# Performance work log

Hardware: AMD Instinct MI355X
Metric: run time of the kernel (lower is better)

Reference implementation:

```python
import jax, jax.numpy as jnp
import numpy as np


def setup_inputs() -> dict:
    key = jax.random.key(0)
    k1, k2, k3, k4 = jax.random.split(key, 4)
    B, I, P, F = 4096, 1024, 512, 2048
    x = jax.random.normal(k1, (B, I), dtype=jnp.float32)
    # params initialized like torch.rand(...)*2-1 (uniform in [-1,1])
    features = jax.random.uniform(k2, (F, I), dtype=jnp.float32, minval=-1.0, maxval=1.0)
    prototypes = jax.random.uniform(k3, (P, I), dtype=jnp.float32, minval=-1.0, maxval=1.0)
    # scalars: torch inits to zeros; use small nonzero values so output/grads are informative
    abt = jax.random.normal(k4, (3,), dtype=jnp.float32) * 0.1
    alpha = abt[0:1]
    beta = abt[1:2]
    theta = abt[2:3]
    return {"x": x, "features": features, "prototypes": prototypes,
            "alpha": alpha, "beta": beta, "theta": theta}


def reference(x, features, prototypes, alpha, beta, theta):
    # x: [b, i], features: [f, i], prototypes: [p, i]
    # Original einsums broadcast over p but the projection is p-independent:
    xf = x @ features.T            # [b, f]
    pf = prototypes @ features.T   # [p, f]
    x_pres = jax.nn.relu(xf)       # [b, f]
    p_pres = jax.nn.relu(pf)       # [p, f]
    # common[b,p]       = sum_f xf*pf*relu(xf)*relu(pf)
    # x_distinct[b,p]   = sum_f xf*relu(xf)*(1-relu(pf))
    # p_distinct[b,p]   = sum_f pf*relu(pf)*(1-relu(xf))
    a = xf * x_pres                # [b, f]
    c = pf * p_pres                # [p, f]
    common = a @ c.T                                   # [b, p]
    x_distinctive = a @ (1.0 - p_pres).T               # [b, p]
    p_distinctive = (1.0 - x_pres) @ c.T               # [b, p]
    return theta * common - alpha * x_distinctive - beta * p_distinctive
```

## Files before the change

### kernel.cpp

```cpp
#include <hip/hip_runtime.h>
#include <cstdint>

typedef __attribute__((ext_vector_type(8))) short bf16x8;
typedef __attribute__((ext_vector_type(4))) float f32x4;
typedef __attribute__((ext_vector_type(4))) float f4;
typedef __attribute__((ext_vector_type(4))) unsigned short u16x4;
typedef __attribute__((ext_vector_type(8))) unsigned short u16x8;
typedef unsigned short u16;

__device__ __forceinline__ u16 f2bf(float f) {
  uint32_t u = __builtin_bit_cast(uint32_t, f);
  u += 0x7fffu + ((u >> 16) & 1u);
  return (u16)(u >> 16);
}

__device__ __forceinline__ void async_cp16(const void* g, void* l) {
  __builtin_amdgcn_global_load_lds(
      (const __attribute__((address_space(1))) uint32_t*)g,
      (__attribute__((address_space(3))) uint32_t*)l, 16, 0, 0);
}

__global__ __launch_bounds__(256) void cast3(
    const float* __restrict__ x, const float* __restrict__ f,
    const float* __restrict__ p, u16* __restrict__ dst,
    int n1, int n2, int n3) {
  int i = (blockIdx.x * 256 + threadIdx.x) * 4;
  const float* src;
  int local;
  if (i < n1) { src = x; local = i; }
  else if (i < n1 + n2) { src = f; local = i - n1; }
  else if (i < n1 + n2 + n3) { src = p; local = i - n1 - n2; }
  else return;
  f4 v = *(const f4*)(src + local);
  u16x4 o;
  o.x = f2bf(v.x); o.y = f2bf(v.y); o.z = f2bf(v.z); o.w = f2bf(v.w);
  *(u16x4*)(dst + i) = o;
}

template<int TM, int TN>
__device__ __forceinline__ void mainloop(
    const u16* __restrict__ A, const u16* __restrict__ B, int K,
    int kbeg, int kend, int tid, u16* lds, f32x4 (&acc)[TM / 32][TN / 32]) {
  constexpr int BK = 64;
  constexpr int WM = TM / 2, WN = TN / 2;
  constexpr int MT = TM / 32, NT = TN / 32;
  const int lane = tid & 63;
  const int wave = tid >> 6;
  const int wrow = wave >> 1, wcol = wave & 1;

  for (int k0 = kbeg; k0 < kend; k0 += BK) {
    #pragma unroll
    for (int it = 0; it < TM / 32; ++it) {
      int c = it * 256 + tid;
      int row = c >> 3, pc = c & 7;
      int gc = pc ^ (row & 7);
      async_cp16(A + (size_t)row * K + (k0 + gc * 8),
                 &lds[(it * 256 + wave * 64) * 8]);
    }
    #pragma unroll
    for (int it = 0; it < TN / 32; ++it) {
      int c = it * 256 + tid;
      int row = c >> 3, pc = c & 7;
      int gc = pc ^ (row & 7);
      async_cp16(B + (size_t)row * K + (k0 + gc * 8),
                 &lds[TM * BK + (it * 256 + wave * 64) * 8]);
    }
    __syncthreads();

    #pragma unroll
    for (int s = 0; s < 2; ++s) {
      const int h = s * 4 + (lane >> 4);
      bf16x8 afr[MT], bfr[NT];
      #pragma unroll
      for (int i = 0; i < MT; ++i) {
        int r = wrow * WM + i * 16 + (lane & 15);
        afr[i] = *(const bf16x8*)&lds[(r * 8 + (h ^ (r & 7))) * 8];
      }
      #pragma unroll
      for (int j = 0; j < NT; ++j) {
        int r = wcol * WN + j * 16 + (lane & 15);
        bfr[j] = *(const bf16x8*)&lds[TM * BK + (r * 8 + (h ^ (r & 7))) * 8];
      }
      #pragma unroll
      for (int i = 0; i < MT; ++i)
        #pragma unroll
        for (int j = 0; j < NT; ++j)
          acc[i][j] = __builtin_amdgcn_mfma_f32_16x16x32_bf16(afr[i], bfr[j], acc[i][j], 0, 0, 0);
    }
    __syncthreads();
  }
}

__global__ __launch_bounds__(256) void gemm12(
    const u16* __restrict__ xb, const u16* __restrict__ pb,
    const u16* __restrict__ fb, u16* __restrict__ Acat, u16* __restrict__ Bcat,
    const float* __restrict__ alpha, const float* __restrict__ beta,
    const float* __restrict__ theta) {
  constexpr int TM = 128, TN = 64, K = 1024, N = 2048;
  constexpr int MT = TM / 32, NT = TN / 32;
  constexpr int TSTRIDE = 72;
  __shared__ u16 lds[(TM + TN) * 64];

  const int tid = threadIdx.x;
  const int lane = tid & 63;
  const int wave = tid >> 6;
  const int wrow = wave >> 1, wcol = wave & 1;
  const int bm_all = blockIdx.x * TM;
  const int bn = blockIdx.y * TN;
  const bool is_x = bm_all < 4096;
  const u16* A = is_x ? xb + (size_t)bm_all * K : pb + (size_t)(bm_all - 4096) * K;
  const u16* B = fb + (size_t)bn * K;

  f32x4 acc[MT][NT] = {};
  mainloop<TM, TN>(A, B, K, 0, K, tid, lds, acc);

  float th = 0.f, al = 0.f, be = 0.f;
  if (!is_x) { th = theta[0]; al = alpha[0]; be = beta[0]; }
  u16* dst = is_x ? Acat : Bcat;
  const int rowbase = is_x ? bm_all : bm_all - 4096;

  #pragma unroll
  for (int half = 0; half < 2; ++half) {
    __syncthreads();
    #pragma unroll
    for (int i = 0; i < MT; ++i) {
      #pragma unroll
      for (int j = 0; j < NT; ++j) {
        const int cl = wcol * 32 + j * 16 + (lane & 15);
        #pragma unroll
        for (int r = 0; r < 4; ++r) {
          const int rl = wrow * 64 + i * 16 + (lane >> 4) * 4 + r;
          float v = acc[i][j][r];
          float pres = v > 0.f ? v : 0.f;
          float o;
          if (is_x) o = half == 0 ? v * pres : 1.f - pres;
          else {
            float cc = v * pres;
            o = half == 0 ? th * cc - al * (1.f - pres) : -be * cc;
          }
          lds[rl * TSTRIDE + cl] = f2bf(o);
        }
      }
    }
    __syncthreads();
    #pragma unroll
    for (int v = 0; v < 4; ++v) {
      const int rl = v * 32 + (tid >> 3);
      const int cl = (tid & 7) * 8;
      u16x8 vec = *(const u16x8*)&lds[rl * TSTRIDE + cl];
      *(u16x8*)&dst[(size_t)(rowbase + rl) * (2 * N) + bn + cl + half * N] = vec;
    }
  }
}

__global__ __launch_bounds__(256) void gemm3(
    const u16* __restrict__ Acat, const u16* __restrict__ Bcat,
    float* __restrict__ part) {
  constexpr int TM = 128, TN = 64, K = 4096, KSPLIT = 4;
  constexpr int MT = TM / 32, NT = TN / 32;
  __shared__ u16 lds[(TM + TN) * 64];

  const int tid = threadIdx.x;
  const int bm = blockIdx.x * TM;
  const int bn = blockIdx.y * TN;
  const int kbeg = blockIdx.z * (K / KSPLIT);
  const int kend = kbeg + (K / KSPLIT);

  f32x4 acc[MT][NT] = {};
  mainloop<TM, TN>(Acat + (size_t)bm * K, Bcat + (size_t)bn * K, K, kbeg, kend,
                   tid, lds, acc);

  const size_t pbase =
      ((size_t)blockIdx.z * 256 + blockIdx.y * 32 + blockIdx.x) * 8192;
  #pragma unroll
  for (int i = 0; i < MT; ++i)
    #pragma unroll
    for (int j = 0; j < NT; ++j)
      *(f4*)&part[pbase + (i * NT + j) * 1024 + tid * 4] = acc[i][j];
}

__global__ __launch_bounds__(256) void reduce4(
    const float* __restrict__ part, float* __restrict__ out) {
  constexpr int N = 512;
  const int tid = threadIdx.x;
  const int lane = tid & 63;
  const int wave = tid >> 6;
  const int wrow = wave >> 1, wcol = wave & 1;
  const int tileId = blockIdx.x;
  const int bm = (tileId & 31) * 128;
  const int bn = (tileId >> 5) * 64;

  #pragma unroll
  for (int s = 0; s < 8; ++s) {
    f4 v = {0.f, 0.f, 0.f, 0.f};
    #pragma unroll
    for (int z = 0; z < 4; ++z)
      v += *(const f4*)&part[((size_t)z * 256 + tileId) * 8192 + s * 1024 + tid * 4];
    const int i = s >> 1, j = s & 1;
    const int gr0 = bm + wrow * 64 + i * 16 + (lane >> 4) * 4;
    const int gc = bn + wcol * 32 + j * 16 + (lane & 15);
    out[(size_t)(gr0 + 0) * N + gc] = v.x;
    out[(size_t)(gr0 + 1) * N + gc] = v.y;
    out[(size_t)(gr0 + 2) * N + gc] = v.z;
    out[(size_t)(gr0 + 3) * N + gc] = v.w;
  }
}

extern "C" void kernel_launch(void* const* d_in, const int* in_sizes, int n_in,
                              void* d_out, int out_size, void* d_ws, size_t ws_size,
                              hipStream_t stream) {
  const float* x     = (const float*)d_in[0];
  const float* feat  = (const float*)d_in[1];
  const float* proto = (const float*)d_in[2];
  const float* alpha = (const float*)d_in[3];
  const float* beta  = (const float*)d_in[4];
  const float* theta = (const float*)d_in[5];
  float* out = (float*)d_out;

  constexpr int Bb = 4096, Ii = 1024, Pp = 512, Ff = 2048;

  char* ws = (char*)d_ws;
  u16* xb    = (u16*)ws;
  u16* fb    = xb + (size_t)Bb * Ii;
  u16* pb    = fb + (size_t)Ff * Ii;
  float* part = (float*)ws;
  size_t r0 = (size_t)4 * 256 * 8192 * 4;
  u16* Acat = (u16*)(ws + r0);
  u16* Bcat = Acat + (size_t)Bb * 2 * Ff;

  const int n1 = Bb * Ii, n2 = Ff * Ii, n3 = Pp * Ii;
  cast3<<<((n1 + n2 + n3) / 4 + 255) / 256, 256, 0, stream>>>(
      x, feat, proto, xb, n1, n2, n3);

  gemm12<<<dim3(36, 32), 256, 0, stream>>>(xb, pb, fb, Acat, Bcat, alpha, beta, theta);

  gemm3<<<dim3(Bb / 128, Pp / 64, 4), 256, 0, stream>>>(Acat, Bcat, part);

  reduce4<<<256, 256, 0, stream>>>(part, out);
}
```

Baseline: 149.7 us.

## Fuse split-K reduction into gemm3 via atomic tile counters; add occupancy hints

Removes the separate reduce4 launch. Each gemm3 block writes its partial tile, then increments a per-tile atomic counter, and the last of the four K-split blocks sums the partials and writes the output. The counters are zeroed inside cast3. Launch-bounds occupancy hints are also added to both GEMM kernels, which may limit registers. The fused path saves one kernel launch and lets the reduction overlap with GEMM work, at the cost of fences and atomics.

```diff
diff --git a/kernel.cpp b/kernel.cpp
--- a/kernel.cpp
+++ b/kernel.cpp
@@ -23,7 +23,8 @@
 __global__ __launch_bounds__(256) void cast3(
     const float* __restrict__ x, const float* __restrict__ f,
     const float* __restrict__ p, u16* __restrict__ dst,
-    int n1, int n2, int n3) {
+    int* __restrict__ cnt, int n1, int n2, int n3) {
+  if (blockIdx.x == 0) cnt[threadIdx.x] = 0;
   int i = (blockIdx.x * 256 + threadIdx.x) * 4;
   const float* src;
   int local;
@@ -91,7 +92,7 @@
   }
 }
 
-__global__ __launch_bounds__(256) void gemm12(
+__global__ __launch_bounds__(256, 5) void gemm12(
     const u16* __restrict__ xb, const u16* __restrict__ pb,
     const u16* __restrict__ fb, u16* __restrict__ Acat, u16* __restrict__ Bcat,
     const float* __restrict__ alpha, const float* __restrict__ beta,
@@ -153,56 +154,58 @@
   }
 }
 
-__global__ __launch_bounds__(256) void gemm3(
+__global__ __launch_bounds__(256, 6) void gemm3(
     const u16* __restrict__ Acat, const u16* __restrict__ Bcat,
-    float* __restrict__ part) {
-  constexpr int TM = 128, TN = 64, K = 4096, KSPLIT = 4;
+    float* __restrict__ part, int* __restrict__ cnt, float* __restrict__ out) {
+  constexpr int TM = 128, TN = 64, K = 4096, N = 512, KSPLIT = 4;
   constexpr int MT = TM / 32, NT = TN / 32;
   __shared__ u16 lds[(TM + TN) * 64];
 
   const int tid = threadIdx.x;
+  const int lane = tid & 63;
+  const int wave = tid >> 6;
+  const int wrow = wave >> 1, wcol = wave & 1;
   const int bm = blockIdx.x * TM;
   const int bn = blockIdx.y * TN;
   const int kbeg = blockIdx.z * (K / KSPLIT);
   const int kend = kbeg + (K / KSPLIT);
+  const int tileId = blockIdx.y * 32 + blockIdx.x;
 
   f32x4 acc[MT][NT] = {};
   mainloop<TM, TN>(Acat + (size_t)bm * K, Bcat + (size_t)bn * K, K, kbeg, kend,
                    tid, lds, acc);
 
-  const size_t pbase =
-      ((size_t)blockIdx.z * 256 + blockIdx.y * 32 + blockIdx.x) * 8192;
   #pragma unroll
   for (int i = 0; i < MT; ++i)
     #pragma unroll
     for (int j = 0; j < NT; ++j)
-      *(f4*)&part[pbase + (i * NT + j) * 1024 + tid * 4] = acc[i][j];
-}
-
-__global__ __launch_bounds__(256) void reduce4(
-    const float* __restrict__ part, float* __restrict__ out) {
-  constexpr int N = 512;
-  const int tid = threadIdx.x;
-  const int lane = tid & 63;
-  const int wave = tid >> 6;
-  const int wrow = wave >> 1, wcol = wave & 1;
-  const int tileId = blockIdx.x;
-  const int bm = (tileId & 31) * 128;
-  const int bn = (tileId >> 5) * 64;
-
-  #pragma unroll
-  for (int s = 0; s < 8; ++s) {
-    f4 v = {0.f, 0.f, 0.f, 0.f};
-    #pragma unroll
-    for (int z = 0; z < 4; ++z)
-      v += *(const f4*)&part[((size_t)z * 256 + tileId) * 8192 + s * 1024 + tid * 4];
-    const int i = s >> 1, j = s & 1;
-    const int gr0 = bm + wrow * 64 + i * 16 + (lane >> 4) * 4;
-    const int gc = bn + wcol * 32 + j * 16 + (lane & 15);
-    out[(size_t)(gr0 + 0) * N + gc] = v.x;
-    out[(size_t)(gr0 + 1) * N + gc] = v.y;
-    out[(size_t)(gr0 + 2) * N + gc] = v.z;
-    out[(size_t)(gr0 + 3) * N + gc] = v.w;
+      *(f4*)&part[((size_t)blockIdx.z * 256 + tileId) * 8192 +
+                  (i * NT + j) * 1024 + tid * 4] = acc[i][j];
+
+  __threadfence();
+  __syncthreads();
+  volatile int* flag = (volatile int*)lds;
+  if (tid == 0) {
+    int prev = atomicAdd(&cnt[tileId], 1);
+    *flag = (prev == KSPLIT - 1) ? 1 : 0;
+  }
+  __syncthreads();
+  if (*flag) {
+    __threadfence();
+    #pragma unroll
+    for (int s = 0; s < 8; ++s) {
+      f4 v = {0.f, 0.f, 0.f, 0.f};
+      #pragma unroll
+      for (int z = 0; z < 4; ++z)
+        v += *(const f4*)&part[((size_t)z * 256 + tileId) * 8192 + s * 1024 + tid * 4];
+      const int i = s >> 1, j = s & 1;
+      const int gr0 = bm + wrow * 64 + i * 16 + (lane >> 4) * 4;
+      const int gc = bn + wcol * 32 + j * 16 + (lane & 15);
+      out[(size_t)(gr0 + 0) * N + gc] = v.x;
+      out[(size_t)(gr0 + 1) * N + gc] = v.y;
+      out[(size_t)(gr0 + 2) * N + gc] = v.z;
+      out[(size_t)(gr0 + 3) * N + gc] = v.w;
+    }
   }
 }
 
@@ -227,14 +230,13 @@
   size_t r0 = (size_t)4 * 256 * 8192 * 4;
   u16* Acat = (u16*)(ws + r0);
   u16* Bcat = Acat + (size_t)Bb * 2 * Ff;
+  int* cnt  = (int*)(Bcat + (size_t)Pp * 2 * Ff);
 
   const int n1 = Bb * Ii, n2 = Ff * Ii, n3 = Pp * Ii;
   cast3<<<((n1 + n2 + n3) / 4 + 255) / 256, 256, 0, stream>>>(
-      x, feat, proto, xb, n1, n2, n3);
+      x, feat, proto, xb, cnt, n1, n2, n3);
 
   gemm12<<<dim3(36, 32), 256, 0, stream>>>(xb, pb, fb, Acat, Bcat, alpha, beta, theta);
 
-  gemm3<<<dim3(Bb / 128, Pp / 64, 4), 256, 0, stream>>>(Acat, Bcat, part);
-
-  reduce4<<<256, 256, 0, stream>>>(part, out);
-}
+  gemm3<<<dim3(Bb / 128, Pp / 64, 4), 256, 0, stream>>>(Acat, Bcat, part, cnt, out);
+}
```

Result: slower. 292.0 us (+95.0%).
